# Kernel optimization log

Measured on AMD Instinct MI355X. Metric: run time of the kernel, lower is better.

Reference implementation:

```python
import jax, jax.numpy as jnp
import numpy as np

B, S, D, H = 8, 1024, 512, 8
HD = D // H
EPS = 1e-5


def layer_norm(x, g, b):
    m = jnp.mean(x, axis=-1, keepdims=True)
    v = jnp.mean(jnp.square(x - m), axis=-1, keepdims=True)
    return (x - m) * jax.lax.rsqrt(v + EPS) * g + b


def mha(x, w_in, b_in, w_out, b_out):
    # x: [B,S,D]; w_in: [3D,D]; PyTorch MultiheadAttention math (no dropout, eval)
    b, s, d = x.shape
    qkv = x @ w_in.T + b_in                      # [B,S,3D]
    q, k, v = jnp.split(qkv, 3, axis=-1)
    q = q.reshape(b, s, H, HD)
    k = k.reshape(b, s, H, HD)
    v = v.reshape(b, s, H, HD)
    scores = jnp.einsum('bqhd,bkhd->bhqk', q, k) / np.sqrt(HD)
    a = jax.nn.softmax(scores, axis=-1)
    o = jnp.einsum('bhqk,bkhd->bqhd', a, v).reshape(b, s, d)
    return o @ w_out.T + b_out


def interp_linear(y, out_size):
    # y: [B,S_in,D]; torch F.interpolate(mode='linear', align_corners=False)
    s_in = y.shape[1]
    scale = s_in / out_size
    src = (jnp.arange(out_size, dtype=jnp.float32) + 0.5) * scale - 0.5
    src = jnp.clip(src, 0.0, s_in - 1.0)
    i0 = jnp.floor(src).astype(jnp.int32)
    i1 = jnp.minimum(i0 + 1, s_in - 1)
    w = (src - i0.astype(jnp.float32))[None, :, None]
    return y[:, i0, :] * (1.0 - w) + y[:, i1, :] * w


def setup_inputs() -> dict:
    key = jax.random.key(0)
    ks = jax.random.split(key, 16)
    sd = 0.02
    return {
        'x': jax.random.normal(ks[0], (B, S, D), jnp.float32),
        'w_in1': jax.random.normal(ks[1], (3 * D, D), jnp.float32) * sd,
        'b_in1': jnp.zeros((3 * D,), jnp.float32),
        'w_out1': jax.random.normal(ks[2], (D, D), jnp.float32) * sd,
        'b_out1': jnp.zeros((D,), jnp.float32),
        'w_in2': jax.random.normal(ks[3], (3 * D, D), jnp.float32) * sd,
        'b_in2': jnp.zeros((3 * D,), jnp.float32),
        'w_out2': jax.random.normal(ks[4], (D, D), jnp.float32) * sd,
        'b_out2': jnp.zeros((D,), jnp.float32),
        'g1': jnp.ones((D,), jnp.float32), 'beta1': jnp.zeros((D,), jnp.float32),
        'g2': jnp.ones((D,), jnp.float32), 'beta2': jnp.zeros((D,), jnp.float32),
        'g3': jnp.ones((D,), jnp.float32), 'beta3': jnp.zeros((D,), jnp.float32),
        'w_ff1': jax.random.normal(ks[5], (4 * D, D), jnp.float32) * sd,
        'b_ff1': jnp.zeros((4 * D,), jnp.float32),
        'w_ff2': jax.random.normal(ks[6], (D, 4 * D), jnp.float32) * sd,
        'b_ff2': jnp.zeros((D,), jnp.float32),
    }


def reference(x, w_in1, b_in1, w_out1, b_out1, w_in2, b_in2, w_out2, b_out2,
              g1, beta1, g2, beta2, g3, beta3, w_ff1, b_ff1, w_ff2, b_ff2):
    a1 = mha(x, w_in1, b_in1, w_out1, b_out1)
    x = layer_norm(x + a1, g1, beta1)
    # avg_pool1d kernel=2 stride=2 ceil_mode (S even -> exact halving)
    pooled = x.reshape(B, S // 2, 2, D).mean(axis=2)
    a2 = mha(pooled, w_in2, b_in2, w_out2, b_out2)
    up = interp_linear(a2, S)
    x = layer_norm(x + up, g2, beta2)
    h = jax.nn.gelu(x @ w_ff1.T + b_ff1, approximate=False)
    ff = h @ w_ff2.T + b_ff2
    return layer_norm(x + ff, g3, beta3)
```

## Files before the change

kernel.cpp:

```cpp
#include <hip/hip_runtime.h>
#include <hip/hip_bf16.h>
#include <math.h>

typedef __hip_bfloat16 bf16;
typedef __attribute__((ext_vector_type(8))) short short8;
typedef __attribute__((ext_vector_type(4))) short s4v;
typedef __attribute__((ext_vector_type(4))) float f32x4;

__device__ __forceinline__ float ldf(const float* p, size_t i) { return p[i]; }
__device__ __forceinline__ float ldf(const bf16*  p, size_t i) { return __bfloat162float(p[i]); }
__device__ __forceinline__ void  stf(float* p, size_t i, float v) { p[i] = v; }
__device__ __forceinline__ void  stf(bf16*  p, size_t i, float v) { p[i] = __float2bfloat16(v); }

__device__ __forceinline__ float ex2(float x) { return __builtin_amdgcn_exp2f(x); }

__device__ __forceinline__ void gl16(const void* gp, void* lp) {
    __builtin_amdgcn_global_load_lds(
        (const __attribute__((address_space(1))) void*)gp,
        (__attribute__((address_space(3))) void*)lp, 16, 0, 0);
}

__global__ __launch_bounds__(256) void cvt_kernel(
    const float* __restrict__ src, bf16* __restrict__ dst, int n)
{
    for (int i = blockIdx.x * 256 + threadIdx.x; i < n; i += gridDim.x * 256)
        dst[i] = __float2bfloat16(src[i]);
}

__global__ __launch_bounds__(256) void cvt_w(
    const float* __restrict__ s0, const float* __restrict__ s1,
    const float* __restrict__ s2, const float* __restrict__ s3,
    const float* __restrict__ s4, const float* __restrict__ s5,
    bf16* __restrict__ dst)
{
    int i = blockIdx.x * 256 + threadIdx.x;
    const float* s; int off;
    if      (i <  786432) { s = s0; off = 0; }
    else if (i < 1048576) { s = s1; off =  786432; }
    else if (i < 1835008) { s = s2; off = 1048576; }
    else if (i < 2097152) { s = s3; off = 1835008; }
    else if (i < 3145728) { s = s4; off = 2097152; }
    else                  { s = s5; off = 3145728; }
    dst[i] = __float2bfloat16(s[i - off]);
}

template <int EPI>
__global__ __launch_bounds__(256) void gemm_mfma(
    const bf16* __restrict__ A, const bf16* __restrict__ W,
    const float* __restrict__ bias, bf16* __restrict__ C,
    int M, int N, int K)
{
    __shared__ __align__(16) bf16 Asl[2][128 * 64];
    __shared__ __align__(16) bf16 Bsl[2][128 * 64];

    const int tid  = threadIdx.x;
    const int lane = tid & 63;
    const int wave = tid >> 6;
    const int wm   = wave >> 1;
    const int wn   = wave & 1;
    const int l15  = lane & 15;
    const int quad = lane >> 4;
    const int sr   = lane >> 3;
    const int sc   = ((lane & 7) ^ sr) * 8;

    const int row0 = blockIdx.y * 128, col0 = blockIdx.x * 128;

    f32x4 acc[4][4] = {};

    const int nk = K >> 6;

    #pragma unroll
    for (int t = 0; t < 4; t++) {
        int r0 = wave * 32 + t * 8;
        gl16(&A[(size_t)(row0 + r0 + sr) * K + sc], &Asl[0][r0 * 64]);
        gl16(&W[(size_t)(col0 + r0 + sr) * K + sc], &Bsl[0][r0 * 64]);
    }

    int cur = 0;
    for (int i = 0; i < nk; i++) {
        __syncthreads();
        if (i + 1 < nk) {
            int k1 = (i + 1) << 6;
            #pragma unroll
            for (int t = 0; t < 4; t++) {
                int r0 = wave * 32 + t * 8;
                gl16(&A[(size_t)(row0 + r0 + sr) * K + k1 + sc], &Asl[cur ^ 1][r0 * 64]);
                gl16(&W[(size_t)(col0 + r0 + sr) * K + k1 + sc], &Bsl[cur ^ 1][r0 * 64]);
            }
        }

        #pragma unroll
        for (int ks = 0; ks < 64; ks += 32) {
            short8 af[4], bfr[4];
            const int g0 = (ks >> 3) + quad;
            const int col = (g0 ^ (l15 & 7)) * 8;
            #pragma unroll
            for (int mt = 0; mt < 4; mt++)
                af[mt] = *(const short8*)&Asl[cur][(wm * 64 + mt * 16 + l15) * 64 + col];
            #pragma unroll
            for (int nt = 0; nt < 4; nt++)
                bfr[nt] = *(const short8*)&Bsl[cur][(wn * 64 + nt * 16 + l15) * 64 + col];
            #pragma unroll
            for (int mt = 0; mt < 4; mt++)
                #pragma unroll
                for (int nt = 0; nt < 4; nt++)
                    acc[mt][nt] = __builtin_amdgcn_mfma_f32_16x16x32_bf16(
                        af[mt], bfr[nt], acc[mt][nt], 0, 0, 0);
        }
        cur ^= 1;
    }

    #pragma unroll
    for (int mt = 0; mt < 4; mt++) {
        int row = row0 + wm * 64 + mt * 16 + quad * 4;
        #pragma unroll
        for (int nt = 0; nt < 4; nt++) {
            int col = col0 + wn * 64 + nt * 16 + l15;
            float bv = bias[col];
            #pragma unroll
            for (int r = 0; r < 4; r++) {
                float v = acc[mt][nt][r] + bv;
                if (EPI == 1) v = 0.5f * v * (1.0f + erff(v * 0.70710678118654752f));
                C[(size_t)(row + r) * N + col] = __float2bfloat16(v);
            }
        }
    }
}

template <int NS>
__global__ __launch_bounds__(256) void flash_attn_mfma(
    const bf16* __restrict__ qkv, bf16* __restrict__ o, int S)
{
    __shared__ __align__(16) bf16 Ks[64 * 72];
    __shared__ __align__(16) bf16 Vt[64 * 68];
    __shared__ __align__(16) bf16 Pl[4][NS * 16 * 72];
    __shared__ float aX[4][NS * 16];

    const int tid = threadIdx.x;
    const int wave = tid >> 6, lane = tid & 63;
    const int l15 = lane & 15, quad = lane >> 4;
    const int q0 = blockIdx.x * (64 * NS), h = blockIdx.y, bb = blockIdx.z;
    const bf16* base = qkv + (size_t)bb * S * 1536 + h * 64;

    short8 qf[NS][2];
    #pragma unroll
    for (int s = 0; s < NS; s++) {
        size_t qoff = (size_t)(q0 + (wave * NS + s) * 16 + l15) * 1536;
        qf[s][0] = *(const short8*)&base[qoff + quad * 8];
        qf[s][1] = *(const short8*)&base[qoff + 32 + quad * 8];
    }

    f32x4 oacc[NS][4] = {};
    float mrow[NS], lrow[NS];
    #pragma unroll
    for (int s = 0; s < NS; s++) { mrow[s] = -3.0e38f; lrow[s] = 0.f; }

    const float CE = 0.18033688f;

    for (int k0 = 0; k0 < S; k0 += 64) {
        __syncthreads();

        #pragma unroll
        for (int t = 0; t < 2; t++) {
            int c = tid + 256 * t;
            int r = c >> 3, col = (c & 7) * 8;
            *(short8*)&Ks[r * 72 + col] =
                *(const short8*)&base[(size_t)(k0 + r) * 1536 + 512 + col];
        }
        #pragma unroll
        for (int i = 0; i < 8; i++) {
            int r = (wave * 8 + i) * 2;
            union { bf16 b[2]; unsigned u; } pk;
            pk.b[0] = base[(size_t)(k0 + r) * 1536 + 1024 + lane];
            pk.b[1] = base[(size_t)(k0 + r + 1) * 1536 + 1024 + lane];
            *(unsigned*)&Vt[lane * 68 + r] = pk.u;
        }
        __syncthreads();

        f32x4 st[NS][4] = {};
        #pragma unroll
        for (int mt = 0; mt < 4; mt++) {
            short8 kf0 = *(const short8*)&Ks[(mt * 16 + l15) * 72 + quad * 8];
            short8 kf1 = *(const short8*)&Ks[(mt * 16 + l15) * 72 + 32 + quad * 8];
            #pragma unroll
            for (int s = 0; s < NS; s++) {
                st[s][mt] = __builtin_amdgcn_mfma_f32_16x16x32_bf16(kf0, qf[s][0], st[s][mt], 0, 0, 0);
                st[s][mt] = __builtin_amdgcn_mfma_f32_16x16x32_bf16(kf1, qf[s][1], st[s][mt], 0, 0, 0);
            }
        }

        #pragma unroll
        for (int s = 0; s < NS; s++) {
            float cm = -3.0e38f;
            #pragma unroll
            for (int mt = 0; mt < 4; mt++)
                #pragma unroll
                for (int r = 0; r < 4; r++) cm = fmaxf(cm, st[s][mt][r]);
            cm = fmaxf(cm, __shfl_xor(cm, 16));
            cm = fmaxf(cm, __shfl_xor(cm, 32));
            float mn = fmaxf(mrow[s], cm);
            float alpha = ex2((mrow[s] - mn) * CE);
            mrow[s] = mn;
            float mb = mn * CE;
            float ps = 0.f;
            #pragma unroll
            for (int mt = 0; mt < 4; mt++) {
                s4v pw;
                #pragma unroll
                for (int r = 0; r < 4; r++) {
                    float p = ex2(st[s][mt][r] * CE - mb);
                    ps += p;
                    union { bf16 b; short h; } cv;
                    cv.b = __float2bfloat16(p);
                    pw[r] = cv.h;
                }
                *(s4v*)&Pl[wave][(s * 16 + l15) * 72 + mt * 16 + quad * 4] = pw;
            }
            ps += __shfl_xor(ps, 16);
            ps += __shfl_xor(ps, 32);
            lrow[s] = lrow[s] * alpha + ps;
            if (quad == 0) aX[wave][s * 16 + l15] = alpha;
        }

        #pragma unroll
        for (int s = 0; s < NS; s++) {
            float a4[4];
            #pragma unroll
            for (int r = 0; r < 4; r++) a4[r] = aX[wave][s * 16 + quad * 4 + r];
            #pragma unroll
            for (int nt = 0; nt < 4; nt++)
                #pragma unroll
                for (int r = 0; r < 4; r++) oacc[s][nt][r] *= a4[r];
        }

        #pragma unroll
        for (int kb = 0; kb < 2; kb++) {
            short8 pf[NS];
            #pragma unroll
            for (int s = 0; s < NS; s++)
                pf[s] = *(const short8*)&Pl[wave][(s * 16 + l15) * 72 + kb * 32 + quad * 8];
            #pragma unroll
            for (int nt = 0; nt < 4; nt++) {
                const bf16* vp = &Vt[(nt * 16 + l15) * 68 + kb * 32 + quad * 8];
                short8 vf;
                *(long*)&vf = *(const long*)vp;
                *((long*)&vf + 1) = *(const long*)(vp + 4);
                #pragma unroll
                for (int s = 0; s < NS; s++)
                    oacc[s][nt] = __builtin_amdgcn_mfma_f32_16x16x32_bf16(pf[s], vf, oacc[s][nt], 0, 0, 0);
            }
        }
    }

    #pragma unroll
    for (int s = 0; s < NS; s++)
        if (quad == 0) aX[wave][s * 16 + l15] = 1.0f / lrow[s];
    #pragma unroll
    for (int s = 0; s < NS; s++) {
        float iv[4];
        #pragma unroll
        for (int r = 0; r < 4; r++) iv[r] = aX[wave][s * 16 + quad * 4 + r];
        #pragma unroll
        for (int nt = 0; nt < 4; nt++)
            #pragma unroll
            for (int r = 0; r < 4; r++) {
                size_t row = (size_t)bb * S + q0 + (wave * NS + s) * 16 + quad * 4 + r;
                o[row * 512 + h * 64 + nt * 16 + l15] = __float2bfloat16(oacc[s][nt][r] * iv[r]);
            }
    }
}

template <typename AT, typename OT, bool INTERP>
__global__ __launch_bounds__(256) void ln_kernel(
    const AT* __restrict__ a, const bf16* __restrict__ bsrc,
    const float* __restrict__ g, const float* __restrict__ beta,
    OT* __restrict__ out)
{
    const int row = blockIdx.x;
    const int t = threadIdx.x;
    const size_t base = (size_t)row * 512;

    float a0 = ldf(a, base + t), a1 = ldf(a, base + t + 256);
    float b0, b1;
    if (INTERP) {
        int s = row & 1023, bb = row >> 10;
        float src = fminf(fmaxf((s + 0.5f) * 0.5f - 0.5f, 0.f), 511.f);
        int i0 = (int)src;
        int i1 = min(i0 + 1, 511);
        float w = src - (float)i0;
        size_t r0 = ((size_t)bb * 512 + i0) * 512;
        size_t r1 = ((size_t)bb * 512 + i1) * 512;
        b0 = __bfloat162float(bsrc[r0 + t]) * (1.f - w) + __bfloat162float(bsrc[r1 + t]) * w;
        b1 = __bfloat162float(bsrc[r0 + t + 256]) * (1.f - w) + __bfloat162float(bsrc[r1 + t + 256]) * w;
    } else {
        b0 = __bfloat162float(bsrc[base + t]);
        b1 = __bfloat162float(bsrc[base + t + 256]);
    }
    float v0 = a0 + b0, v1 = a1 + b1;

    __shared__ float red[4];
    const int lane = t & 63, wid = t >> 6;

    float sm = v0 + v1;
    #pragma unroll
    for (int off = 32; off > 0; off >>= 1) sm += __shfl_xor(sm, off);
    if (lane == 0) red[wid] = sm;
    __syncthreads();
    sm = red[0] + red[1] + red[2] + red[3];
    const float mean = sm * (1.0f / 512.0f);

    float d0 = v0 - mean, d1 = v1 - mean;
    float vv = d0 * d0 + d1 * d1;
    __syncthreads();
    #pragma unroll
    for (int off = 32; off > 0; off >>= 1) vv += __shfl_xor(vv, off);
    if (lane == 0) red[wid] = vv;
    __syncthreads();
    vv = red[0] + red[1] + red[2] + red[3];
    const float rstd = rsqrtf(vv * (1.0f / 512.0f) + 1e-5f);

    stf(out, base + t,       d0 * rstd * g[t]       + beta[t]);
    stf(out, base + t + 256, d1 * rstd * g[t + 256] + beta[t + 256]);
}

__global__ __launch_bounds__(256) void pool_kernel(
    const bf16* __restrict__ x, bf16* __restrict__ p)
{
    size_t i = (size_t)blockIdx.x * 256 + threadIdx.x;
    size_t d = i & 511;
    size_t rs = i >> 9;
    size_t b = rs >> 9, s = rs & 511;
    size_t r = (b * 1024 + 2 * s) * 512 + d;
    p[i] = __float2bfloat16(0.5f * (__bfloat162float(x[r]) + __bfloat162float(x[r + 512])));
}

extern "C" void kernel_launch(void* const* d_in, const int* in_sizes, int n_in,
                              void* d_out, int out_size, void* d_ws, size_t ws_size,
                              hipStream_t stream)
{
    const float* x      = (const float*)d_in[0];
    const float* w_in1  = (const float*)d_in[1];
    const float* b_in1  = (const float*)d_in[2];
    const float* w_out1 = (const float*)d_in[3];
    const float* b_out1 = (const float*)d_in[4];
    const float* w_in2  = (const float*)d_in[5];
    const float* b_in2  = (const float*)d_in[6];
    const float* w_out2 = (const float*)d_in[7];
    const float* b_out2 = (const float*)d_in[8];
    const float* g1     = (const float*)d_in[9];
    const float* be1    = (const float*)d_in[10];
    const float* g2     = (const float*)d_in[11];
    const float* be2    = (const float*)d_in[12];
    const float* g3     = (const float*)d_in[13];
    const float* be3    = (const float*)d_in[14];
    const float* w_ff1  = (const float*)d_in[15];
    const float* b_ff1  = (const float*)d_in[16];
    const float* w_ff2  = (const float*)d_in[17];
    const float* b_ff2  = (const float*)d_in[18];

    bf16* ws     = (bf16*)d_ws;
    bf16* xb     = ws + 0;
    bf16* wq1    = ws + 4194304;
    bf16* wo1    = ws + 4980736;
    bf16* wq2    = ws + 5242880;
    bf16* wo2    = ws + 6029312;
    bf16* wf1    = ws + 6291456;
    bf16* wf2    = ws + 7340032;
    bf16* qkv1   = ws + 8388608;
    bf16* o1     = ws + 20971520;
    bf16* a1     = ws + 25165824;
    bf16* x1     = ws + 29360128;
    bf16* pooled = ws + 33554432;
    bf16* qkv2   = ws + 35651584;
    bf16* o2     = ws + 41943040;
    bf16* a2     = ws + 44040192;
    bf16* x2     = ws + 46137344;
    bf16* h      = ws + 8388608;
    bf16* ff     = ws + 25165824;

    dim3 blk(256);

    cvt_kernel<<<4096, blk, 0, stream>>>(x, xb, 4194304);
    cvt_w<<<16384, blk, 0, stream>>>(w_in1, w_out1, w_in2, w_out2, w_ff1, w_ff2, wq1);

    gemm_mfma<0><<<dim3(12, 64), blk, 0, stream>>>(xb, wq1, b_in1, qkv1, 8192, 1536, 512);
    flash_attn_mfma<2><<<dim3(8, 8, 8), blk, 0, stream>>>(qkv1, o1, 1024);
    gemm_mfma<0><<<dim3(4, 64), blk, 0, stream>>>(o1, wo1, b_out1, a1, 8192, 512, 512);
    ln_kernel<float, bf16, false><<<8192, blk, 0, stream>>>(x, a1, g1, be1, x1);
    pool_kernel<<<8192, blk, 0, stream>>>(x1, pooled);
    gemm_mfma<0><<<dim3(12, 32), blk, 0, stream>>>(pooled, wq2, b_in2, qkv2, 4096, 1536, 512);
    flash_attn_mfma<1><<<dim3(8, 8, 8), blk, 0, stream>>>(qkv2, o2, 512);
    gemm_mfma<0><<<dim3(4, 32), blk, 0, stream>>>(o2, wo2, b_out2, a2, 4096, 512, 512);
    ln_kernel<bf16, bf16, true><<<8192, blk, 0, stream>>>(x1, a2, g2, be2, x2);
    gemm_mfma<1><<<dim3(16, 64), blk, 0, stream>>>(x2, wf1, b_ff1, h, 8192, 2048, 512);
    gemm_mfma<0><<<dim3(4, 64), blk, 0, stream>>>(h, wf2, b_ff2, ff, 8192, 512, 2048);
    ln_kernel<bf16, float, false><<<8192, blk, 0, stream>>>(x2, ff, g3, be3, (float*)d_out);
}
```

Measured before the change: 338.9 us.

## Restructure flash attention: register-prefetch K/V, lazy rescale, XCD-aware block mapping

Rewrites the attention kernel so each block handles 64 queries with one 16-row tile per wave, and prefetches the next K/V tile into registers while the current tile is computed. V is loaded as vectorized 4-element chunks and transposed into LDS with 8-byte stores instead of scalar gathers. The online softmax now skips the output rescale unless the running max rises by more than a threshold, and alpha is broadcast by shuffles rather than through LDS. Blocks are launched on a 1D grid remapped so neighbouring (batch, head) work lands on the same XCD for L2 reuse. In exchange, the first attention's block count doubles, so each K/V tile is loaded and staged by twice as many blocks.

New measurement: 338.1 us. Within noise of the previous version (-0.2%).

```diff
diff --git a/kernel.cpp b/kernel.cpp
--- a/kernel.cpp
+++ b/kernel.cpp
@@ -127,147 +127,160 @@
     }
 }
 
-template <int NS>
+template <int LQ>
 __global__ __launch_bounds__(256) void flash_attn_mfma(
-    const bf16* __restrict__ qkv, bf16* __restrict__ o, int S)
+    const bf16* __restrict__ qkv, bf16* __restrict__ o)
 {
     __shared__ __align__(16) bf16 Ks[64 * 72];
     __shared__ __align__(16) bf16 Vt[64 * 68];
-    __shared__ __align__(16) bf16 Pl[4][NS * 16 * 72];
-    __shared__ float aX[4][NS * 16];
-
-    const int tid = threadIdx.x;
+    __shared__ __align__(16) bf16 Pl[4][16 * 72];
+
+    const int S   = 64 << LQ;
+    const int nQB = 1 << LQ;
+
+    const int tid  = threadIdx.x;
     const int wave = tid >> 6, lane = tid & 63;
-    const int l15 = lane & 15, quad = lane >> 4;
-    const int q0 = blockIdx.x * (64 * NS), h = blockIdx.y, bb = blockIdx.z;
+    const int l15  = lane & 15, quad = lane >> 4;
+
+    const int r    = blockIdx.x;
+    const int w    = (r & 7) * (8 << LQ) + (r >> 3);
+    const int qblk = w & (nQB - 1);
+    const int bh   = w >> LQ;
+    const int h    = bh & 7, bb = bh >> 3;
+    const int q0   = qblk * 64;
+
     const bf16* base = qkv + (size_t)bb * S * 1536 + h * 64;
 
-    short8 qf[NS][2];
-    #pragma unroll
-    for (int s = 0; s < NS; s++) {
-        size_t qoff = (size_t)(q0 + (wave * NS + s) * 16 + l15) * 1536;
-        qf[s][0] = *(const short8*)&base[qoff + quad * 8];
-        qf[s][1] = *(const short8*)&base[qoff + 32 + quad * 8];
-    }
-
-    f32x4 oacc[NS][4] = {};
-    float mrow[NS], lrow[NS];
-    #pragma unroll
-    for (int s = 0; s < NS; s++) { mrow[s] = -3.0e38f; lrow[s] = 0.f; }
-
+    short8 qf[2];
+    {
+        size_t qoff = (size_t)(q0 + wave * 16 + l15) * 1536;
+        qf[0] = *(const short8*)&base[qoff + quad * 8];
+        qf[1] = *(const short8*)&base[qoff + 32 + quad * 8];
+    }
+
+    f32x4 oacc[4] = {};
+    float m2 = -3.0e38f, lrow = 0.f;
     const float CE = 0.18033688f;
 
-    for (int k0 = 0; k0 < S; k0 += 64) {
-        __syncthreads();
-
+    short8 kst[2];
+    s4v    vst[4];
+    const int vr4 = (tid >> 4) * 4;
+    const int vc0 = (tid & 15) * 4;
+
+    auto LOADK = [&](int k0) {
         #pragma unroll
         for (int t = 0; t < 2; t++) {
             int c = tid + 256 * t;
-            int r = c >> 3, col = (c & 7) * 8;
-            *(short8*)&Ks[r * 72 + col] =
-                *(const short8*)&base[(size_t)(k0 + r) * 1536 + 512 + col];
-        }
-        #pragma unroll
-        for (int i = 0; i < 8; i++) {
-            int r = (wave * 8 + i) * 2;
-            union { bf16 b[2]; unsigned u; } pk;
-            pk.b[0] = base[(size_t)(k0 + r) * 1536 + 1024 + lane];
-            pk.b[1] = base[(size_t)(k0 + r + 1) * 1536 + 1024 + lane];
-            *(unsigned*)&Vt[lane * 68 + r] = pk.u;
-        }
+            int rr = c >> 3, col = (c & 7) * 8;
+            kst[t] = *(const short8*)&base[(size_t)(k0 + rr) * 1536 + 512 + col];
+        }
+        #pragma unroll
+        for (int rr = 0; rr < 4; rr++)
+            vst[rr] = *(const s4v*)&base[(size_t)(k0 + vr4 + rr) * 1536 + 1024 + vc0];
+    };
+
+    auto WRITEKV = [&]() {
+        #pragma unroll
+        for (int t = 0; t < 2; t++) {
+            int c = tid + 256 * t;
+            int rr = c >> 3, col = (c & 7) * 8;
+            *(short8*)&Ks[rr * 72 + col] = kst[t];
+        }
+        #pragma unroll
+        for (int i = 0; i < 4; i++) {
+            union { bf16 b[4]; unsigned u[2]; } pk;
+            pk.b[0] = ((const bf16*)&vst[0])[i];
+            pk.b[1] = ((const bf16*)&vst[1])[i];
+            pk.b[2] = ((const bf16*)&vst[2])[i];
+            pk.b[3] = ((const bf16*)&vst[3])[i];
+            *(unsigned long long*)&Vt[(vc0 + i) * 68 + vr4] =
+                *(const unsigned long long*)pk.u;
+        }
+    };
+
+    LOADK(0);
+    const int nt = 1 << LQ;
+    for (int it = 0; it < nt; it++) {
         __syncthreads();
-
-        f32x4 st[NS][4] = {};
+        WRITEKV();
+        __syncthreads();
+        if (it + 1 < nt) LOADK((it + 1) << 6);
+
+        f32x4 st[4] = {};
         #pragma unroll
         for (int mt = 0; mt < 4; mt++) {
             short8 kf0 = *(const short8*)&Ks[(mt * 16 + l15) * 72 + quad * 8];
             short8 kf1 = *(const short8*)&Ks[(mt * 16 + l15) * 72 + 32 + quad * 8];
-            #pragma unroll
-            for (int s = 0; s < NS; s++) {
-                st[s][mt] = __builtin_amdgcn_mfma_f32_16x16x32_bf16(kf0, qf[s][0], st[s][mt], 0, 0, 0);
-                st[s][mt] = __builtin_amdgcn_mfma_f32_16x16x32_bf16(kf1, qf[s][1], st[s][mt], 0, 0, 0);
+            st[mt] = __builtin_amdgcn_mfma_f32_16x16x32_bf16(kf0, qf[0], st[mt], 0, 0, 0);
+            st[mt] = __builtin_amdgcn_mfma_f32_16x16x32_bf16(kf1, qf[1], st[mt], 0, 0, 0);
+        }
+
+        float cm = -3.0e38f;
+        #pragma unroll
+        for (int mt = 0; mt < 4; mt++)
+            #pragma unroll
+            for (int rr = 0; rr < 4; rr++) cm = fmaxf(cm, st[mt][rr]);
+        cm = fmaxf(cm, __shfl_xor(cm, 16));
+        cm = fmaxf(cm, __shfl_xor(cm, 32));
+        float cm2 = cm * CE;
+
+        if (__any(cm2 > m2 + 8.f)) {
+            float mn2   = fmaxf(m2, cm2);
+            float alpha = ex2(m2 - mn2);
+            m2 = mn2;
+            lrow *= alpha;
+            float a4[4];
+            #pragma unroll
+            for (int rr = 0; rr < 4; rr++) a4[rr] = __shfl(alpha, quad * 4 + rr);
+            #pragma unroll
+            for (int ntt = 0; ntt < 4; ntt++)
+                #pragma unroll
+                for (int rr = 0; rr < 4; rr++) oacc[ntt][rr] *= a4[rr];
+        }
+
+        float ps = 0.f;
+        #pragma unroll
+        for (int mt = 0; mt < 4; mt++) {
+            s4v pw;
+            #pragma unroll
+            for (int rr = 0; rr < 4; rr++) {
+                float p = ex2(st[mt][rr] * CE - m2);
+                ps += p;
+                union { bf16 b; short hh; } cv;
+                cv.b = __float2bfloat16(p);
+                pw[rr] = cv.hh;
             }
-        }
-
-        #pragma unroll
-        for (int s = 0; s < NS; s++) {
-            float cm = -3.0e38f;
-            #pragma unroll
-            for (int mt = 0; mt < 4; mt++)
-                #pragma unroll
-                for (int r = 0; r < 4; r++) cm = fmaxf(cm, st[s][mt][r]);
-            cm = fmaxf(cm, __shfl_xor(cm, 16));
-            cm = fmaxf(cm, __shfl_xor(cm, 32));
-            float mn = fmaxf(mrow[s], cm);
-            float alpha = ex2((mrow[s] - mn) * CE);
-            mrow[s] = mn;
-            float mb = mn * CE;
-            float ps = 0.f;
-            #pragma unroll
-            for (int mt = 0; mt < 4; mt++) {
-                s4v pw;
-                #pragma unroll
-                for (int r = 0; r < 4; r++) {
-                    float p = ex2(st[s][mt][r] * CE - mb);
-                    ps += p;
-                    union { bf16 b; short h; } cv;
-                    cv.b = __float2bfloat16(p);
-                    pw[r] = cv.h;
-                }
-                *(s4v*)&Pl[wave][(s * 16 + l15) * 72 + mt * 16 + quad * 4] = pw;
+            *(s4v*)&Pl[wave][l15 * 72 + mt * 16 + quad * 4] = pw;
+        }
+        ps += __shfl_xor(ps, 16);
+        ps += __shfl_xor(ps, 32);
+        lrow += ps;
+
+        #pragma unroll
+        for (int kb = 0; kb < 2; kb++) {
+            short8 pf = *(const short8*)&Pl[wave][l15 * 72 + kb * 32 + quad * 8];
+            #pragma unroll
+            for (int ntt = 0; ntt < 4; ntt++) {
+                const bf16* vp = &Vt[(ntt * 16 + l15) * 68 + kb * 32 + quad * 8];
+                short8 vf;
+                *(unsigned long long*)&vf       = *(const unsigned long long*)vp;
+                *((unsigned long long*)&vf + 1) = *(const unsigned long long*)(vp + 4);
+                oacc[ntt] = __builtin_amdgcn_mfma_f32_16x16x32_bf16(pf, vf, oacc[ntt], 0, 0, 0);
             }
-            ps += __shfl_xor(ps, 16);
-            ps += __shfl_xor(ps, 32);
-            lrow[s] = lrow[s] * alpha + ps;
-            if (quad == 0) aX[wave][s * 16 + l15] = alpha;
-        }
-
-        #pragma unroll
-        for (int s = 0; s < NS; s++) {
-            float a4[4];
-            #pragma unroll
-            for (int r = 0; r < 4; r++) a4[r] = aX[wave][s * 16 + quad * 4 + r];
-            #pragma unroll
-            for (int nt = 0; nt < 4; nt++)
-                #pragma unroll
-                for (int r = 0; r < 4; r++) oacc[s][nt][r] *= a4[r];
-        }
-
-        #pragma unroll
-        for (int kb = 0; kb < 2; kb++) {
-            short8 pf[NS];
-            #pragma unroll
-            for (int s = 0; s < NS; s++)
-                pf[s] = *(const short8*)&Pl[wave][(s * 16 + l15) * 72 + kb * 32 + quad * 8];
-            #pragma unroll
-            for (int nt = 0; nt < 4; nt++) {
-                const bf16* vp = &Vt[(nt * 16 + l15) * 68 + kb * 32 + quad * 8];
-                short8 vf;
-                *(long*)&vf = *(const long*)vp;
-                *((long*)&vf + 1) = *(const long*)(vp + 4);
-                #pragma unroll
-                for (int s = 0; s < NS; s++)
-                    oacc[s][nt] = __builtin_amdgcn_mfma_f32_16x16x32_bf16(pf[s], vf, oacc[s][nt], 0, 0, 0);
-            }
-        }
-    }
-
-    #pragma unroll
-    for (int s = 0; s < NS; s++)
-        if (quad == 0) aX[wave][s * 16 + l15] = 1.0f / lrow[s];
-    #pragma unroll
-    for (int s = 0; s < NS; s++) {
-        float iv[4];
-        #pragma unroll
-        for (int r = 0; r < 4; r++) iv[r] = aX[wave][s * 16 + quad * 4 + r];
-        #pragma unroll
-        for (int nt = 0; nt < 4; nt++)
-            #pragma unroll
-            for (int r = 0; r < 4; r++) {
-                size_t row = (size_t)bb * S + q0 + (wave * NS + s) * 16 + quad * 4 + r;
-                o[row * 512 + h * 64 + nt * 16 + l15] = __float2bfloat16(oacc[s][nt][r] * iv[r]);
-            }
-    }
+        }
+    }
+
+    float inv = 1.0f / lrow;
+    float iv[4];
+    #pragma unroll
+    for (int rr = 0; rr < 4; rr++) iv[rr] = __shfl(inv, quad * 4 + rr);
+    #pragma unroll
+    for (int ntt = 0; ntt < 4; ntt++)
+        #pragma unroll
+        for (int rr = 0; rr < 4; rr++) {
+            size_t row = (size_t)bb * S + q0 + wave * 16 + quad * 4 + rr;
+            o[row * 512 + h * 64 + ntt * 16 + l15] = __float2bfloat16(oacc[ntt][rr] * iv[rr]);
+        }
 }
 
 template <typename AT, typename OT, bool INTERP>
@@ -384,12 +397,12 @@
     cvt_w<<<16384, blk, 0, stream>>>(w_in1, w_out1, w_in2, w_out2, w_ff1, w_ff2, wq1);
 
     gemm_mfma<0><<<dim3(12, 64), blk, 0, stream>>>(xb, wq1, b_in1, qkv1, 8192, 1536, 512);
-    flash_attn_mfma<2><<<dim3(8, 8, 8), blk, 0, stream>>>(qkv1, o1, 1024);
+    flash_attn_mfma<4><<<dim3(1024), blk, 0, stream>>>(qkv1, o1);
     gemm_mfma<0><<<dim3(4, 64), blk, 0, stream>>>(o1, wo1, b_out1, a1, 8192, 512, 512);
     ln_kernel<float, bf16, false><<<8192, blk, 0, stream>>>(x, a1, g1, be1, x1);
     pool_kernel<<<8192, blk, 0, stream>>>(x1, pooled);
     gemm_mfma<0><<<dim3(12, 32), blk, 0, stream>>>(pooled, wq2, b_in2, qkv2, 4096, 1536, 512);
-    flash_attn_mfma<1><<<dim3(8, 8, 8), blk, 0, stream>>>(qkv2, o2, 512);
+    flash_attn_mfma<3><<<dim3(512), blk, 0, stream>>>(qkv2, o2);
     gemm_mfma<0><<<dim3(4, 32), blk, 0, stream>>>(o2, wo2, b_out2, a2, 4096, 512, 512);
     ln_kernel<bf16, bf16, true><<<8192, blk, 0, stream>>>(x1, a2, g2, be2, x2);
     gemm_mfma<1><<<dim3(16, 64), blk, 0, stream>>>(x2, wf1, b_ff1, h, 8192, 2048, 512);
```
